# Kernel optimization log

Measured on AMD Instinct MI355X. Metric: run time of the kernel, lower is better.

## Reference

```python
import jax, jax.numpy as jnp
import numpy as np

B, S, D_MODEL, D_STATE = 4, 2048, 2048, 64
C = 8.0
SURPRISE_TEMP = 1.0
RMS_EPS = 1e-6


def _l2norm(x, eps=1e-12):
    # F.normalize(dim=-1): x / max(||x||_2, eps)
    n = jnp.sqrt(jnp.sum(x * x, axis=-1, keepdims=True))
    return x / jnp.maximum(n, eps)


def setup_inputs() -> dict:
    key = jax.random.key(0)
    ks = jax.random.split(key, 9)
    std = 0.02
    return {
        "x": jax.random.normal(ks[0], (B, S, D_MODEL), dtype=jnp.float32),
        "Wk": jax.random.normal(ks[1], (D_STATE, D_MODEL), dtype=jnp.float32) * std,
        "Wv": jax.random.normal(ks[2], (D_STATE, D_MODEL), dtype=jnp.float32) * std,
        "Wq": jax.random.normal(ks[3], (D_STATE, D_MODEL), dtype=jnp.float32) * std,
        "Wa_w": jax.random.normal(ks[4], (D_STATE, D_MODEL), dtype=jnp.float32) * std,
        "Wa_b": jnp.zeros((D_STATE,), dtype=jnp.float32),
        "lam": jax.random.uniform(ks[5], (D_STATE,), dtype=jnp.float32, minval=4.0, maxval=9.0),
        "norm_w": jnp.ones((D_STATE,), dtype=jnp.float32),
        "Wo": jax.random.normal(ks[6], (D_MODEL, D_STATE), dtype=jnp.float32) * std,
    }


def reference(x, Wk, Wv, Wq, Wa_w, Wa_b, lam, norm_w, Wo):
    b, s, _ = x.shape
    d = Wk.shape[0]
    # projections
    k = _l2norm(x @ Wk.T)                    # [B,S,d]
    v = x @ Wv.T                             # [B,S,d]
    q = _l2norm(x @ Wq.T)                    # [B,S,d]
    r = jax.nn.sigmoid(x @ Wa_w.T + Wa_b)    # [B,S,d]
    log_a = jnp.log(jax.nn.sigmoid(lam) + 1e-8)
    alpha = jnp.exp(C * r * log_a)           # [B,S,d]

    def step(H, inp):
        # H: [B, d_k, d_v]; inp tensors: [B, d]
        k_t, v_t, q_t, a_t = inp
        pred = jnp.einsum("bk,bkv->bv", q_t, H)
        err = jnp.sum((v_t - pred) ** 2, axis=-1, keepdims=True)   # [B,1]
        surprise = jax.nn.sigmoid(err / (SURPRISE_TEMP + 1e-6))    # [B,1]
        kH = jnp.einsum("bk,bkv->bv", k_t, H)
        # delta = k (x) v - k (x) (k^T H) = k (x) (v - kH)
        delta = k_t[:, :, None] * (v_t - kH)[:, None, :]           # [B,d,d]
        a = a_t[:, :, None]                                        # gate over k-dim rows
        H = a * H + (1.0 - a) * (surprise[:, :, None] * delta)
        y_t = jnp.einsum("bk,bkv->bv", q_t, H)
        return H, y_t

    H0 = jnp.zeros((b, d, d), dtype=x.dtype)
    xs = (
        jnp.swapaxes(k, 0, 1),
        jnp.swapaxes(v, 0, 1),
        jnp.swapaxes(q, 0, 1),
        jnp.swapaxes(alpha, 0, 1),
    )
    _, ys = jax.lax.scan(step, H0, xs)       # ys: [S,B,d]
    y = jnp.swapaxes(ys, 0, 1)               # [B,S,d]

    # RMSNorm (computed in fp32, cast back)
    yf = y.astype(jnp.float32)
    yn = yf * jax.lax.rsqrt(jnp.mean(yf * yf, axis=-1, keepdims=True) + RMS_EPS)
    yn = (yn * norm_w).astype(y.dtype)

    return yn @ Wo.T                          # [B,S,d_model]
```

## Files before the change

kernel.cpp:

```cpp
#include <hip/hip_runtime.h>
#include <hip/hip_bf16.h>
#include <math.h>

#define S_ 2048
#define DM_ 2048

__device__ __forceinline__ float wave_reduce_add_f32(float x) {
  float t;
  t = __int_as_float(__builtin_amdgcn_update_dpp(0, __float_as_int(x), 0x111, 0xf, 0xf, true)); x += t;
  t = __int_as_float(__builtin_amdgcn_update_dpp(0, __float_as_int(x), 0x112, 0xf, 0xf, true)); x += t;
  t = __int_as_float(__builtin_amdgcn_update_dpp(0, __float_as_int(x), 0x114, 0xf, 0xf, true)); x += t;
  t = __int_as_float(__builtin_amdgcn_update_dpp(0, __float_as_int(x), 0x118, 0xf, 0xf, true)); x += t;
  t = __int_as_float(__builtin_amdgcn_update_dpp(0, __float_as_int(x), 0x142, 0xa, 0xf, true)); x += t;
  t = __int_as_float(__builtin_amdgcn_update_dpp(0, __float_as_int(x), 0x143, 0xc, 0xf, true)); x += t;
  return __int_as_float(__builtin_amdgcn_readlane(__float_as_int(x), 63));
}

__global__ __launch_bounds__(256) void k_proj(
    const float* __restrict__ x, const float* __restrict__ Wk,
    const float* __restrict__ Wv, const float* __restrict__ Wq,
    const float* __restrict__ Wa, const float* __restrict__ Wab,
    const float* __restrict__ lam, float* __restrict__ proj,
    float* __restrict__ qwArr)
{
  __shared__ __align__(16) float xs[16 * 40];
  __shared__ __align__(16) float ws[32 * 260];
  const int tid = threadIdx.x;
  const int r0  = blockIdx.x * 16;
  const int ct  = tid & 63;
  const int rt  = tid >> 6;
  float acc[4][4];
  #pragma unroll
  for (int r = 0; r < 4; r++) { acc[r][0] = 0.f; acc[r][1] = 0.f; acc[r][2] = 0.f; acc[r][3] = 0.f; }

  const int sg = tid >> 3;
  const int sm = tid & 7;
  const float* wbase[4] = {Wk, Wv, Wq, Wa};

  for (int k0 = 0; k0 < DM_; k0 += 32) {
    if (tid < 128) {
      const int rr = tid >> 3;
      const int ko = (tid & 7) << 2;
      float4 xv = *(const float4*)(x + (size_t)(r0 + rr) * DM_ + k0 + ko);
      *(float4*)(xs + rr * 40 + ko) = xv;
    }
    #pragma unroll
    for (int p = 0; p < 8; p++) {
      const int c = sg + p * 32;
      const float* wb = wbase[p >> 1];
      const int cc = c - (p >> 1) * 64;
      float4 wv = *(const float4*)(wb + (size_t)cc * DM_ + k0 + sm * 4);
      ws[(sm * 4 + 0) * 260 + c] = wv.x;
      ws[(sm * 4 + 1) * 260 + c] = wv.y;
      ws[(sm * 4 + 2) * 260 + c] = wv.z;
      ws[(sm * 4 + 3) * 260 + c] = wv.w;
    }
    __syncthreads();
    #pragma unroll
    for (int kq = 0; kq < 8; kq++) {
      float4 xv[4];
      #pragma unroll
      for (int r = 0; r < 4; r++) xv[r] = *(const float4*)(xs + (rt * 4 + r) * 40 + kq * 4);
      #pragma unroll
      for (int i = 0; i < 4; i++) {
        const int kk = kq * 4 + i;
        float wv0 = ws[kk * 260 + ct];
        float wv1 = ws[kk * 260 + ct + 64];
        float wv2 = ws[kk * 260 + ct + 128];
        float wv3 = ws[kk * 260 + ct + 192];
        #pragma unroll
        for (int r = 0; r < 4; r++) {
          float xr = (i == 0) ? xv[r].x : (i == 1) ? xv[r].y : (i == 2) ? xv[r].z : xv[r].w;
          acc[r][0] = fmaf(xr, wv0, acc[r][0]);
          acc[r][1] = fmaf(xr, wv1, acc[r][1]);
          acc[r][2] = fmaf(xr, wv2, acc[r][2]);
          acc[r][3] = fmaf(xr, wv3, acc[r][3]);
        }
      }
    }
    __syncthreads();
  }
  float lamv = lam[ct];
  float la = logf(1.f / (1.f + expf(-lamv)) + 1e-8f);
  float bv = Wab[ct];
  #pragma unroll
  for (int r = 0; r < 4; r++) {
    float nk = wave_reduce_add_f32(acc[r][0] * acc[r][0]);
    float nq = wave_reduce_add_f32(acc[r][2] * acc[r][2]);
    nk = fmaxf(sqrtf(nk), 1e-12f);
    nq = fmaxf(sqrtf(nq), 1e-12f);
    float pre = acc[r][3] + bv;
    float rr_ = 1.f / (1.f + expf(-pre));
    float al  = expf(8.f * rr_ * la);
    float kn  = acc[r][0] / nk;
    float qn  = acc[r][2] / nq;
    float qw  = wave_reduce_add_f32(qn * (1.f - al) * kn);
    float* pr = proj + (size_t)(r0 + rt * 4 + r) * 256;
    pr[ct]        = kn;
    pr[64 + ct]   = acc[r][1];
    pr[128 + ct]  = qn;
    pr[192 + ct]  = al;
    if (ct == 0) qwArr[r0 + rt * 4 + r] = qw;
  }
}

struct KQA { float4 k[4], q[4], a[4]; float v; };

__device__ __forceinline__ void load_kqa(const float* __restrict__ slot,
                                         int w, int lane, KQA& s) {
  const float4* s4 = (const float4*)slot;
  const int o = w * 4;
  #pragma unroll
  for (int i = 0; i < 4; i++) {
    s.k[i] = s4[o + i];
    s.q[i] = s4[32 + o + i];
    s.a[i] = s4[48 + o + i];
  }
  s.v = slot[64 + lane];
}

__device__ __forceinline__ void sstep(int t, float qws, float* __restrict__ inv,
    float2* __restrict__ xchp, float* __restrict__ yb, const float* __restrict__ pb,
    float H[16], KQA& cur, KQA& nxt, float& pf, int w, int lane, int tid,
    float qwSel)
{
  inv[(((t + 2) & 3) << 8) + tid] = pf;
  pf = pb[(size_t)min(t + 4, S_ - 1) * 256 + tid];
  float4 w4[4], qa4[4];
  #pragma unroll
  for (int j = 0; j < 4; j++) {
    w4[j].x = (1.f - cur.a[j].x) * cur.k[j].x;  qa4[j].x = cur.q[j].x * cur.a[j].x;
    w4[j].y = (1.f - cur.a[j].y) * cur.k[j].y;  qa4[j].y = cur.q[j].y * cur.a[j].y;
    w4[j].z = (1.f - cur.a[j].z) * cur.k[j].z;  qa4[j].z = cur.q[j].z * cur.a[j].z;
    w4[j].w = (1.f - cur.a[j].w) * cur.k[j].w;  qa4[j].w = cur.q[j].w * cur.a[j].w;
  }
  float pA = 0.f, pB = 0.f, kA = 0.f, kB = 0.f, yA = 0.f, yB = 0.f;
  #pragma unroll
  for (int j = 0; j < 4; j++) {
    pA = fmaf(cur.q[j].x, H[4*j+0], pA); kA = fmaf(cur.k[j].x, H[4*j+0], kA); yA = fmaf(qa4[j].x, H[4*j+0], yA);
    pB = fmaf(cur.q[j].y, H[4*j+1], pB); kB = fmaf(cur.k[j].y, H[4*j+1], kB); yB = fmaf(qa4[j].y, H[4*j+1], yB);
    pA = fmaf(cur.q[j].z, H[4*j+2], pA); kA = fmaf(cur.k[j].z, H[4*j+2], kA); yA = fmaf(qa4[j].z, H[4*j+2], yA);
    pB = fmaf(cur.q[j].w, H[4*j+3], pB); kB = fmaf(cur.k[j].w, H[4*j+3], kB); yB = fmaf(qa4[j].w, H[4*j+3], yB);
  }
  xchp[(w << 6) + lane] = make_float2(pA + pB, kA + kB);
  asm volatile("s_waitcnt lgkmcnt(0)\n\ts_barrier" ::: "memory");
  float2 x0 = xchp[lane], x1 = xchp[64 + lane], x2 = xchp[128 + lane], x3 = xchp[192 + lane];
  load_kqa(inv + (((t + 1) & 3) << 8), w, lane, nxt);
  float pred = (x0.x + x1.x) + (x2.x + x3.x);
  float kh   = (x0.y + x1.y) + (x2.y + x3.y);
  float d = cur.v - pred;
  float e = wave_reduce_add_f32(d * d);
  float sg = __builtin_amdgcn_rcpf(1.f + __builtin_amdgcn_exp2f(e * -1.4426936f));
  float g = sg * (cur.v - kh);
  yb[(size_t)t * 256 + (w << 6) + lane] = (yA + yB) + qwSel * (qws * g);
  #pragma unroll
  for (int j = 0; j < 4; j++) {
    H[4*j+0] = fmaf(cur.a[j].x, H[4*j+0], w4[j].x * g);
    H[4*j+1] = fmaf(cur.a[j].y, H[4*j+1], w4[j].y * g);
    H[4*j+2] = fmaf(cur.a[j].z, H[4*j+2], w4[j].z * g);
    H[4*j+3] = fmaf(cur.a[j].w, H[4*j+3], w4[j].w * g);
  }
}

__global__ __launch_bounds__(256, 1) void k_scan(const float* __restrict__ proj,
    const float* __restrict__ qwArr, float* __restrict__ ypart)
{
  __shared__ __align__(16) float inv[4 * 256];
  __shared__ __align__(16) float2 xch[2][256];
  const int b = blockIdx.x, tid = threadIdx.x;
  const int w = tid >> 6, lane = tid & 63;
  const float* pb  = proj + (size_t)b * S_ * 256;
  const float* qwb = qwArr + (size_t)b * S_;
  float* yb = ypart + (size_t)b * S_ * 256;
  float H[16];
  #pragma unroll
  for (int j = 0; j < 16; j++) H[j] = 0.f;
  inv[tid]       = pb[tid];
  inv[256 + tid] = pb[256 + tid];
  float pfE = pb[2 * 256 + tid];
  float pfO = pb[3 * 256 + tid];
  __syncthreads();
  const float qwSel = (w == 0) ? 1.f : 0.f;
  KQA curA, curB;
  load_kqa(inv, w, lane, curA);
  for (int t0 = 0; t0 < S_; t0 += 64) {
    float qwv = qwb[t0 + lane];
    for (int tt = 0; tt < 64; tt += 2) {
      float qs0 = __int_as_float(__builtin_amdgcn_readlane(__float_as_int(qwv), tt));
      float qs1 = __int_as_float(__builtin_amdgcn_readlane(__float_as_int(qwv), tt + 1));
      sstep(t0 + tt,     qs0, inv, xch[0], yb, pb, H, curA, curB, pfE, w, lane, tid, qwSel);
      sstep(t0 + tt + 1, qs1, inv, xch[1], yb, pb, H, curB, curA, pfO, w, lane, tid, qwSel);
    }
  }
}

__global__ __launch_bounds__(256) void k_trans(const float* __restrict__ Wo,
                                               float* __restrict__ WoT) {
  int i = blockIdx.x * 256 + threadIdx.x;
  int d = i >> 11;
  int c = i & 2047;
  WoT[i] = Wo[(size_t)c * 64 + d];
}

__global__ __launch_bounds__(256) void k_out(const float* __restrict__ ypart,
    const float* __restrict__ norm_w, const float* __restrict__ WoT,
    float* __restrict__ out)
{
  __shared__ __align__(16) float yn[16 * 64];
  const int tid = threadIdx.x;
  const int r0  = blockIdx.x * 16;
  const int c0  = blockIdx.y * 512;
  {
    const int r = tid >> 4;
    const int d = (tid & 15) * 4;
    const float* yp = ypart + (size_t)(r0 + r) * 256;
    float4 y0 = *(const float4*)(yp + d);
    float4 y1 = *(const float4*)(yp + 64 + d);
    float4 y2 = *(const float4*)(yp + 128 + d);
    float4 y3 = *(const float4*)(yp + 192 + d);
    float yx = y0.x + y1.x + y2.x + y3.x;
    float yy = y0.y + y1.y + y2.y + y3.y;
    float yz = y0.z + y1.z + y2.z + y3.z;
    float yw = y0.w + y1.w + y2.w + y3.w;
    float sq = yx * yx + yy * yy + yz * yz + yw * yw;
    sq += __shfl_xor(sq, 1, 64);
    sq += __shfl_xor(sq, 2, 64);
    sq += __shfl_xor(sq, 4, 64);
    sq += __shfl_xor(sq, 8, 64);
    float rms = rsqrtf(sq * (1.f / 64.f) + 1e-6f);
    float4 nw = *(const float4*)(norm_w + d);
    yn[r * 64 + d + 0] = yx * rms * nw.x;
    yn[r * 64 + d + 1] = yy * rms * nw.y;
    yn[r * 64 + d + 2] = yz * rms * nw.z;
    yn[r * 64 + d + 3] = yw * rms * nw.w;
  }
  __syncthreads();
  const int ctq = tid & 127;
  const int rt  = tid >> 7;
  float acc[8][4];
  #pragma unroll
  for (int r = 0; r < 8; r++) { acc[r][0] = 0.f; acc[r][1] = 0.f; acc[r][2] = 0.f; acc[r][3] = 0.f; }
  #pragma unroll 8
  for (int d = 0; d < 64; d++) {
    float4 wv = *(const float4*)(WoT + (size_t)d * 2048 + c0 + ctq * 4);
    #pragma unroll
    for (int r = 0; r < 8; r++) {
      float yv = yn[(rt * 8 + r) * 64 + d];
      acc[r][0] = fmaf(yv, wv.x, acc[r][0]);
      acc[r][1] = fmaf(yv, wv.y, acc[r][1]);
      acc[r][2] = fmaf(yv, wv.z, acc[r][2]);
      acc[r][3] = fmaf(yv, wv.w, acc[r][3]);
    }
  }
  #pragma unroll
  for (int r = 0; r < 8; r++) {
    float4 o; o.x = acc[r][0]; o.y = acc[r][1]; o.z = acc[r][2]; o.w = acc[r][3];
    *(float4*)(out + (size_t)(r0 + rt * 8 + r) * 2048 + c0 + ctq * 4) = o;
  }
}

extern "C" void kernel_launch(void* const* d_in, const int* in_sizes, int n_in,
                              void* d_out, int out_size, void* d_ws, size_t ws_size,
                              hipStream_t stream) {
  const float* x   = (const float*)d_in[0];
  const float* Wk  = (const float*)d_in[1];
  const float* Wv  = (const float*)d_in[2];
  const float* Wq  = (const float*)d_in[3];
  const float* Wa  = (const float*)d_in[4];
  const float* Wab = (const float*)d_in[5];
  const float* lam = (const float*)d_in[6];
  const float* nw  = (const float*)d_in[7];
  const float* Wo  = (const float*)d_in[8];
  float* out = (float*)d_out;

  float* wsf   = (float*)d_ws;
  float* proj  = wsf;
  float* ypart = wsf + 2097152;
  float* WoT   = wsf + 4194304;
  float* qwArr = wsf + 4325376;

  k_trans<<<dim3(512), dim3(256), 0, stream>>>(Wo, WoT);
  k_proj <<<dim3(512), dim3(256), 0, stream>>>(x, Wk, Wv, Wq, Wa, Wab, lam, proj, qwArr);
  k_scan <<<dim3(4),   dim3(256), 0, stream>>>(proj, qwArr, ypart);
  k_out  <<<dim3(512, 4), dim3(256), 0, stream>>>(ypart, nw, WoT, out);
}
```

Baseline: 1.375 ms.

## Precompute next-step dot products to take H update off the serial critical path

Rewrites the scan recurrence so that the q·H, k·H and output dot products for step t+1 are computed from the pre-update state H_t, using the next step's gates. The rank-1 correction from the current step's update is applied as scalar coefficients that a new k_coef kernel precomputes per timestep. The intent is to shorten the per-step dependency chain in the latency-bound 4-block scan, so the cross-wave exchange and barrier overlap with the state update. In exchange it adds an extra kernel launch, more FMAs per step and an algebraic reordering that can change rounding.

```diff
diff --git a/kernel.cpp b/kernel.cpp
--- a/kernel.cpp
+++ b/kernel.cpp
@@ -14,6 +14,10 @@
   t = __int_as_float(__builtin_amdgcn_update_dpp(0, __float_as_int(x), 0x142, 0xa, 0xf, true)); x += t;
   t = __int_as_float(__builtin_amdgcn_update_dpp(0, __float_as_int(x), 0x143, 0xc, 0xf, true)); x += t;
   return __int_as_float(__builtin_amdgcn_readlane(__float_as_int(x), 63));
+}
+
+__device__ __forceinline__ float rdlane(float x, int l) {
+  return __int_as_float(__builtin_amdgcn_readlane(__float_as_int(x), l));
 }
 
 __global__ __launch_bounds__(256) void k_proj(
@@ -104,6 +108,29 @@
   }
 }
 
+__global__ __launch_bounds__(256) void k_coef(const float* __restrict__ proj,
+                                              float* __restrict__ scArr)
+{
+  const int row  = blockIdx.x * 4 + (threadIdx.x >> 6);
+  const int lane = threadIdx.x & 63;
+  const int t = row & (S_ - 1);
+  const float* pr = proj + (size_t)row * 256;
+  float kn = pr[lane];
+  float qn = pr[128 + lane];
+  float al = pr[192 + lane];
+  float wprev = 0.f;
+  if (t > 0) {
+    const float* pp = pr - 256;
+    wprev = (1.f - pp[192 + lane]) * pp[lane];
+  }
+  float w  = (1.f - al) * kn;
+  float cq = wave_reduce_add_f32(qn * wprev);
+  float ck = wave_reduce_add_f32(kn * wprev);
+  float cy = wave_reduce_add_f32(qn * al * wprev);
+  float qw = wave_reduce_add_f32(qn * w);
+  if (lane == 0) *(float4*)(scArr + (size_t)row * 4) = make_float4(cq, ck, cy, qw);
+}
+
 struct KQA { float4 k[4], q[4], a[4]; float v; };
 
 __device__ __forceinline__ void load_kqa(const float* __restrict__ slot,
@@ -119,62 +146,70 @@
   s.v = slot[64 + lane];
 }
 
-__device__ __forceinline__ void sstep(int t, float qws, float* __restrict__ inv,
-    float2* __restrict__ xchp, float* __restrict__ yb, const float* __restrict__ pb,
-    float H[16], KQA& cur, KQA& nxt, float& pf, int w, int lane, int tid,
-    float qwSel)
-{
-  inv[(((t + 2) & 3) << 8) + tid] = pf;
-  pf = pb[(size_t)min(t + 4, S_ - 1) * 256 + tid];
-  float4 w4[4], qa4[4];
-  #pragma unroll
-  for (int j = 0; j < 4; j++) {
-    w4[j].x = (1.f - cur.a[j].x) * cur.k[j].x;  qa4[j].x = cur.q[j].x * cur.a[j].x;
-    w4[j].y = (1.f - cur.a[j].y) * cur.k[j].y;  qa4[j].y = cur.q[j].y * cur.a[j].y;
-    w4[j].z = (1.f - cur.a[j].z) * cur.k[j].z;  qa4[j].z = cur.q[j].z * cur.a[j].z;
-    w4[j].w = (1.f - cur.a[j].w) * cur.k[j].w;  qa4[j].w = cur.q[j].w * cur.a[j].w;
-  }
-  float pA = 0.f, pB = 0.f, kA = 0.f, kB = 0.f, yA = 0.f, yB = 0.f;
-  #pragma unroll
-  for (int j = 0; j < 4; j++) {
-    pA = fmaf(cur.q[j].x, H[4*j+0], pA); kA = fmaf(cur.k[j].x, H[4*j+0], kA); yA = fmaf(qa4[j].x, H[4*j+0], yA);
-    pB = fmaf(cur.q[j].y, H[4*j+1], pB); kB = fmaf(cur.k[j].y, H[4*j+1], kB); yB = fmaf(qa4[j].y, H[4*j+1], yB);
-    pA = fmaf(cur.q[j].z, H[4*j+2], pA); kA = fmaf(cur.k[j].z, H[4*j+2], kA); yA = fmaf(qa4[j].z, H[4*j+2], yA);
-    pB = fmaf(cur.q[j].w, H[4*j+3], pB); kB = fmaf(cur.k[j].w, H[4*j+3], kB); yB = fmaf(qa4[j].w, H[4*j+3], yB);
-  }
-  xchp[(w << 6) + lane] = make_float2(pA + pB, kA + kB);
-  asm volatile("s_waitcnt lgkmcnt(0)\n\ts_barrier" ::: "memory");
-  float2 x0 = xchp[lane], x1 = xchp[64 + lane], x2 = xchp[128 + lane], x3 = xchp[192 + lane];
-  load_kqa(inv + (((t + 1) & 3) << 8), w, lane, nxt);
-  float pred = (x0.x + x1.x) + (x2.x + x3.x);
-  float kh   = (x0.y + x1.y) + (x2.y + x3.y);
+__device__ __forceinline__ void sstep(int t, float4 sc, float* __restrict__ inv,
+    const float2* __restrict__ xchR, float2* __restrict__ xchW,
+    float* __restrict__ yb, const float* __restrict__ pb,
+    float H[16], KQA& cur, KQA& nxt, float& d3c, float& gP,
+    float& pf, int w, int lane, int tid, float qwSel)
+{
+  float2 x0 = xchR[lane], x1 = xchR[64 + lane], x2 = xchR[128 + lane], x3 = xchR[192 + lane];
+  float D1f = (x0.x + x1.x) + (x2.x + x3.x);
+  float D2f = (x0.y + x1.y) + (x2.y + x3.y);
+  float pred = fmaf(sc.x, gP, D1f);
+  float kh   = fmaf(sc.y, gP, D2f);
   float d = cur.v - pred;
   float e = wave_reduce_add_f32(d * d);
   float sg = __builtin_amdgcn_rcpf(1.f + __builtin_amdgcn_exp2f(e * -1.4426936f));
   float g = sg * (cur.v - kh);
-  yb[(size_t)t * 256 + (w << 6) + lane] = (yA + yB) + qwSel * (qws * g);
+  yb[(size_t)t * 256 + tid] = d3c + qwSel * fmaf(sc.z, gP, sc.w * g);
+  inv[(((t + 2) & 3) << 8) + tid] = pf;
+  pf = pb[(size_t)min(t + 4, S_ - 1) * 256 + tid];
+  load_kqa(inv + (((t + 1) & 3) << 8), w, lane, nxt);
+  float dA = 0.f, dB = 0.f, kA = 0.f, kB = 0.f, yA = 0.f, yB = 0.f;
   #pragma unroll
   for (int j = 0; j < 4; j++) {
-    H[4*j+0] = fmaf(cur.a[j].x, H[4*j+0], w4[j].x * g);
-    H[4*j+1] = fmaf(cur.a[j].y, H[4*j+1], w4[j].y * g);
-    H[4*j+2] = fmaf(cur.a[j].z, H[4*j+2], w4[j].z * g);
-    H[4*j+3] = fmaf(cur.a[j].w, H[4*j+3], w4[j].w * g);
-  }
+    float c1, c2, c3;
+    c1 = nxt.q[j].x * cur.a[j].x; c2 = nxt.k[j].x * cur.a[j].x; c3 = c1 * nxt.a[j].x;
+    dA = fmaf(c1, H[4*j+0], dA); kA = fmaf(c2, H[4*j+0], kA); yA = fmaf(c3, H[4*j+0], yA);
+    c1 = nxt.q[j].y * cur.a[j].y; c2 = nxt.k[j].y * cur.a[j].y; c3 = c1 * nxt.a[j].y;
+    dB = fmaf(c1, H[4*j+1], dB); kB = fmaf(c2, H[4*j+1], kB); yB = fmaf(c3, H[4*j+1], yB);
+    c1 = nxt.q[j].z * cur.a[j].z; c2 = nxt.k[j].z * cur.a[j].z; c3 = c1 * nxt.a[j].z;
+    dA = fmaf(c1, H[4*j+2], dA); kA = fmaf(c2, H[4*j+2], kA); yA = fmaf(c3, H[4*j+2], yA);
+    c1 = nxt.q[j].w * cur.a[j].w; c2 = nxt.k[j].w * cur.a[j].w; c3 = c1 * nxt.a[j].w;
+    dB = fmaf(c1, H[4*j+3], dB); kB = fmaf(c2, H[4*j+3], kB); yB = fmaf(c3, H[4*j+3], yB);
+  }
+  d3c = yA + yB;
+  xchW[(w << 6) + lane] = make_float2(dA + dB, kA + kB);
+  #pragma unroll
+  for (int j = 0; j < 4; j++) {
+    float wx = (1.f - cur.a[j].x) * cur.k[j].x;
+    float wy = (1.f - cur.a[j].y) * cur.k[j].y;
+    float wz = (1.f - cur.a[j].z) * cur.k[j].z;
+    float ww = (1.f - cur.a[j].w) * cur.k[j].w;
+    H[4*j+0] = fmaf(cur.a[j].x, H[4*j+0], wx * g);
+    H[4*j+1] = fmaf(cur.a[j].y, H[4*j+1], wy * g);
+    H[4*j+2] = fmaf(cur.a[j].z, H[4*j+2], wz * g);
+    H[4*j+3] = fmaf(cur.a[j].w, H[4*j+3], ww * g);
+  }
+  asm volatile("s_waitcnt lgkmcnt(0)\n\ts_barrier" ::: "memory");
+  gP = g;
 }
 
 __global__ __launch_bounds__(256, 1) void k_scan(const float* __restrict__ proj,
-    const float* __restrict__ qwArr, float* __restrict__ ypart)
+    const float* __restrict__ scArr, float* __restrict__ ypart)
 {
   __shared__ __align__(16) float inv[4 * 256];
   __shared__ __align__(16) float2 xch[2][256];
   const int b = blockIdx.x, tid = threadIdx.x;
   const int w = tid >> 6, lane = tid & 63;
   const float* pb  = proj + (size_t)b * S_ * 256;
-  const float* qwb = qwArr + (size_t)b * S_;
+  const float4* scb = (const float4*)scArr + (size_t)b * S_;
   float* yb = ypart + (size_t)b * S_ * 256;
   float H[16];
   #pragma unroll
   for (int j = 0; j < 16; j++) H[j] = 0.f;
+  float gP = 0.f, d3c = 0.f;
+  xch[0][tid] = make_float2(0.f, 0.f);
   inv[tid]       = pb[tid];
   inv[256 + tid] = pb[256 + tid];
   float pfE = pb[2 * 256 + tid];
@@ -184,12 +219,14 @@
   KQA curA, curB;
   load_kqa(inv, w, lane, curA);
   for (int t0 = 0; t0 < S_; t0 += 64) {
-    float qwv = qwb[t0 + lane];
+    float4 scv = scb[t0 + lane];
     for (int tt = 0; tt < 64; tt += 2) {
-      float qs0 = __int_as_float(__builtin_amdgcn_readlane(__float_as_int(qwv), tt));
-      float qs1 = __int_as_float(__builtin_amdgcn_readlane(__float_as_int(qwv), tt + 1));
-      sstep(t0 + tt,     qs0, inv, xch[0], yb, pb, H, curA, curB, pfE, w, lane, tid, qwSel);
-      sstep(t0 + tt + 1, qs1, inv, xch[1], yb, pb, H, curB, curA, pfO, w, lane, tid, qwSel);
+      float4 s0 = make_float4(rdlane(scv.x, tt),     rdlane(scv.y, tt),
+                              rdlane(scv.z, tt),     rdlane(scv.w, tt));
+      float4 s1 = make_float4(rdlane(scv.x, tt + 1), rdlane(scv.y, tt + 1),
+                              rdlane(scv.z, tt + 1), rdlane(scv.w, tt + 1));
+      sstep(t0 + tt,     s0, inv, xch[0], xch[1], yb, pb, H, curA, curB, d3c, gP, pfE, w, lane, tid, qwSel);
+      sstep(t0 + tt + 1, s1, inv, xch[1], xch[0], yb, pb, H, curB, curA, d3c, gP, pfO, w, lane, tid, qwSel);
     }
   }
 }
@@ -278,9 +315,11 @@
   float* ypart = wsf + 2097152;
   float* WoT   = wsf + 4194304;
   float* qwArr = wsf + 4325376;
+  float* scArr = wsf + 4333568;
 
   k_trans<<<dim3(512), dim3(256), 0, stream>>>(Wo, WoT);
   k_proj <<<dim3(512), dim3(256), 0, stream>>>(x, Wk, Wv, Wq, Wa, Wab, lam, proj, qwArr);
-  k_scan <<<dim3(4),   dim3(256), 0, stream>>>(proj, qwArr, ypart);
+  k_coef <<<dim3(2048), dim3(256), 0, stream>>>(proj, scArr);
+  k_scan <<<dim3(4),   dim3(256), 0, stream>>>(proj, scArr, ypart);
   k_out  <<<dim3(512, 4), dim3(256), 0, stream>>>(ypart, nw, WoT, out);
 }
```

Result: slower. 1.524 ms (+10.9%).

## Process two scan steps per barrier using precomputed cross-step coefficients

Applied to the files above, without the earlier changes.

Restructures the sequential delta-rule scan to advance two timesteps per block barrier instead of one. A new k_coef kernel precomputes scalar dot-product coefficients between adjacent steps' k/q/a rows, so the dependence of step t+1 on the not-yet-applied updates of step t (and of the previous pair) is folded in algebraically. The cost targeted is the per-step barrier and shared-memory exchange latency on the serial critical path. In exchange there is an extra kernel launch, more FMAs per thread per step, an 8-slot input ring, and the results may differ slightly in floating-point rounding.

```diff
diff --git a/kernel.cpp b/kernel.cpp
--- a/kernel.cpp
+++ b/kernel.cpp
@@ -4,6 +4,7 @@
 
 #define S_ 2048
 #define DM_ 2048
+#define NPH (S_ / 2)
 
 __device__ __forceinline__ float wave_reduce_add_f32(float x) {
   float t;
@@ -104,93 +105,181 @@
   }
 }
 
-struct KQA { float4 k[4], q[4], a[4]; float v; };
-
-__device__ __forceinline__ void load_kqa(const float* __restrict__ slot,
-                                         int w, int lane, KQA& s) {
-  const float4* s4 = (const float4*)slot;
+__global__ __launch_bounds__(256) void k_coef(const float* __restrict__ proj,
+                                              float* __restrict__ scArr)
+{
+  const int P    = blockIdx.x * 4 + (threadIdx.x >> 6);
+  const int lane = threadIdx.x & 63;
+  const int p    = P & (NPH - 1);
+  const int t    = p * 2;
+  const float* pr0 = proj + ((size_t)(P >> 10) * S_ + t) * 256;
+  const float* pr1 = pr0 + 256;
+  float k0 = pr0[lane], q0 = pr0[128 + lane], a0 = pr0[192 + lane];
+  float k1 = pr1[lane], q1 = pr1[128 + lane], a1 = pr1[192 + lane];
+  float w0 = (1.f - a0) * k0;
+  float w1 = (1.f - a1) * k1;
+  float W0p = 0.f, W1p = 0.f;
+  if (p > 0) {
+    const float* pm1 = pr0 - 256;
+    const float* pm2 = pr0 - 512;
+    float am1 = pm1[192 + lane], km1 = pm1[lane];
+    float am2 = pm2[192 + lane], km2 = pm2[lane];
+    float wm2 = (1.f - am2) * km2;
+    W0p = am1 * wm2;
+    W1p = (1.f - am1) * km1;
+  }
+  float q0a0 = q0 * a0;
+  float q1a0 = q1 * a0;
+  float k1a0 = k1 * a0;
+  float q1a1a0 = q1a0 * a1;
+  float sq00 = wave_reduce_add_f32(q0 * W0p);
+  float sq01 = wave_reduce_add_f32(q0 * W1p);
+  float sk00 = wave_reduce_add_f32(k0 * W0p);
+  float sk01 = wave_reduce_add_f32(k0 * W1p);
+  float sy00 = wave_reduce_add_f32(q0a0 * W0p);
+  float sy01 = wave_reduce_add_f32(q0a0 * W1p);
+  float qw0  = wave_reduce_add_f32(q0 * w0);
+  float sq10 = wave_reduce_add_f32(q1a0 * W0p);
+  float sq11 = wave_reduce_add_f32(q1a0 * W1p);
+  float sk10 = wave_reduce_add_f32(k1a0 * W0p);
+  float sk11 = wave_reduce_add_f32(k1a0 * W1p);
+  float sy10 = wave_reduce_add_f32(q1a1a0 * W0p);
+  float sy11 = wave_reduce_add_f32(q1a1a0 * W1p);
+  float cqi  = wave_reduce_add_f32(q1 * w0);
+  float cki  = wave_reduce_add_f32(k1 * w0);
+  float cyi  = wave_reduce_add_f32(q1 * a1 * w0);
+  float qw1  = wave_reduce_add_f32(q1 * w1);
+  if (lane == 0) {
+    float4* so = (float4*)(scArr + (size_t)P * 20);
+    so[0] = make_float4(sq00, sq01, sk00, sk01);
+    so[1] = make_float4(sy00, sy01, qw0, sq10);
+    so[2] = make_float4(sq11, sk10, sk11, sy10);
+    so[3] = make_float4(sy11, cqi, cki, cyi);
+    so[4] = make_float4(qw1, 0.f, 0.f, 0.f);
+  }
+}
+
+struct Rows { float4 q[2][4], k[2][4], a[2][4]; };
+
+__device__ __forceinline__ void load_rows(const float* __restrict__ inv,
+                                          int sA, int sB, int w, Rows& R) {
+  const float4* r0 = (const float4*)(inv + (sA << 8));
+  const float4* r1 = (const float4*)(inv + (sB << 8));
   const int o = w * 4;
   #pragma unroll
   for (int i = 0; i < 4; i++) {
-    s.k[i] = s4[o + i];
-    s.q[i] = s4[32 + o + i];
-    s.a[i] = s4[48 + o + i];
-  }
-  s.v = slot[64 + lane];
-}
-
-__device__ __forceinline__ void sstep(int t, float qws, float* __restrict__ inv,
-    float2* __restrict__ xchp, float* __restrict__ yb, const float* __restrict__ pb,
-    float H[16], KQA& cur, KQA& nxt, float& pf, int w, int lane, int tid,
-    float qwSel)
-{
-  inv[(((t + 2) & 3) << 8) + tid] = pf;
-  pf = pb[(size_t)min(t + 4, S_ - 1) * 256 + tid];
-  float4 w4[4], qa4[4];
+    R.k[0][i] = r0[o + i];       R.k[1][i] = r1[o + i];
+    R.q[0][i] = r0[32 + o + i];  R.q[1][i] = r1[32 + o + i];
+    R.a[0][i] = r0[48 + o + i];  R.a[1][i] = r1[48 + o + i];
+  }
+}
+
+#define PHASE_DOT(J, C, HI) { \
+  float A_  = CUR.a[1][J].C * CUR.a[0][J].C; \
+  float c1_ = NXT.q[0][J].C * A_; \
+  float c2_ = NXT.k[0][J].C * A_; \
+  float c3_ = c1_ * NXT.a[0][J].C; \
+  float am_ = NXT.a[0][J].C * A_; \
+  float f1_ = NXT.q[1][J].C * am_; \
+  float f2_ = NXT.k[1][J].C * am_; \
+  float f3_ = f1_ * NXT.a[1][J].C; \
+  float h_  = H[4*(J)+(HI)]; \
+  D1n = fmaf(c1_, h_, D1n); D2n = fmaf(c2_, h_, D2n); D3n = fmaf(c3_, h_, D3n); \
+  D1m = fmaf(f1_, h_, D1m); D2m = fmaf(f2_, h_, D2m); D3m = fmaf(f3_, h_, D3m); }
+
+#define PHASE_HUP(J, C, HI) { \
+  float a0_ = CUR.a[0][J].C, a1_ = CUR.a[1][J].C; \
+  float w0_ = (1.f - a0_) * CUR.k[0][J].C; \
+  float w1_ = (1.f - a1_) * CUR.k[1][J].C; \
+  float tm_ = fmaf(w1_, g1, (a1_ * w0_) * g0); \
+  H[4*(J)+(HI)] = fmaf(a1_ * a0_, H[4*(J)+(HI)], tm_); }
+
+__device__ __forceinline__ void pstep(int t,
+    const float4* __restrict__ sc, float4* __restrict__ scn,
+    const float4* __restrict__ scb,
+    float* __restrict__ inv, const float4* __restrict__ xchR,
+    float4* __restrict__ xchW, float* __restrict__ yb,
+    const float* __restrict__ pb, float H[16], Rows& CUR, Rows& NXT,
+    float& d3c0, float& d3c1, float& g0p, float& g1p,
+    float& pfE, float& pfO, int w, int lane, int tid, float qwSel)
+{
+  {
+    const float4* sp = scb + (size_t)min((t >> 1) + 1, NPH - 1) * 5;
+    scn[0] = sp[0]; scn[1] = sp[1]; scn[2] = sp[2]; scn[3] = sp[3]; scn[4] = sp[4];
+  }
+  float v0 = inv[((t & 7) << 8) + 64 + lane];
+  float v1 = inv[(((t + 1) & 7) << 8) + 64 + lane];
+  load_rows(inv, (t + 2) & 7, (t + 3) & 7, w, NXT);
+  float4 x0 = xchR[lane], x1 = xchR[64 + lane], x2 = xchR[128 + lane], x3 = xchR[192 + lane];
+  float D1  = (x0.x + x1.x) + (x2.x + x3.x);
+  float D2  = (x0.y + x1.y) + (x2.y + x3.y);
+  float D1b = (x0.z + x1.z) + (x2.z + x3.z);
+  float D2b = (x0.w + x1.w) + (x2.w + x3.w);
+  float pred0 = fmaf(sc[0].x, g0p, fmaf(sc[0].y, g1p, D1));
+  float kh0   = fmaf(sc[0].z, g0p, fmaf(sc[0].w, g1p, D2));
+  float d0 = v0 - pred0;
+  float e0 = wave_reduce_add_f32(d0 * d0);
+  float sg0 = __builtin_amdgcn_rcpf(1.f + __builtin_amdgcn_exp2f(e0 * -1.4426936f));
+  float g0 = sg0 * (v0 - kh0);
+  yb[(size_t)t * 256 + tid] = d3c0 + qwSel * fmaf(sc[1].x, g0p, fmaf(sc[1].y, g1p, sc[1].z * g0));
+  float pred1 = fmaf(sc[3].y, g0, fmaf(sc[1].w, g0p, fmaf(sc[2].x, g1p, D1b)));
+  float kh1   = fmaf(sc[3].z, g0, fmaf(sc[2].y, g0p, fmaf(sc[2].z, g1p, D2b)));
+  float d1 = v1 - pred1;
+  float e1 = wave_reduce_add_f32(d1 * d1);
+  float sg1 = __builtin_amdgcn_rcpf(1.f + __builtin_amdgcn_exp2f(e1 * -1.4426936f));
+  float g1 = sg1 * (v1 - kh1);
+  yb[(size_t)(t + 1) * 256 + tid] =
+      d3c1 + qwSel * fmaf(sc[2].w, g0p, fmaf(sc[3].x, g1p, fmaf(sc[3].w, g0, sc[4].x * g1)));
+  float D1n = 0.f, D2n = 0.f, D3n = 0.f, D1m = 0.f, D2m = 0.f, D3m = 0.f;
   #pragma unroll
   for (int j = 0; j < 4; j++) {
-    w4[j].x = (1.f - cur.a[j].x) * cur.k[j].x;  qa4[j].x = cur.q[j].x * cur.a[j].x;
-    w4[j].y = (1.f - cur.a[j].y) * cur.k[j].y;  qa4[j].y = cur.q[j].y * cur.a[j].y;
-    w4[j].z = (1.f - cur.a[j].z) * cur.k[j].z;  qa4[j].z = cur.q[j].z * cur.a[j].z;
-    w4[j].w = (1.f - cur.a[j].w) * cur.k[j].w;  qa4[j].w = cur.q[j].w * cur.a[j].w;
-  }
-  float pA = 0.f, pB = 0.f, kA = 0.f, kB = 0.f, yA = 0.f, yB = 0.f;
+    PHASE_DOT(j, x, 0); PHASE_DOT(j, y, 1); PHASE_DOT(j, z, 2); PHASE_DOT(j, w, 3);
+  }
+  d3c0 = D3n;
+  d3c1 = D3m;
+  xchW[(w << 6) + lane] = make_float4(D1n, D2n, D1m, D2m);
   #pragma unroll
   for (int j = 0; j < 4; j++) {
-    pA = fmaf(cur.q[j].x, H[4*j+0], pA); kA = fmaf(cur.k[j].x, H[4*j+0], kA); yA = fmaf(qa4[j].x, H[4*j+0], yA);
-    pB = fmaf(cur.q[j].y, H[4*j+1], pB); kB = fmaf(cur.k[j].y, H[4*j+1], kB); yB = fmaf(qa4[j].y, H[4*j+1], yB);
-    pA = fmaf(cur.q[j].z, H[4*j+2], pA); kA = fmaf(cur.k[j].z, H[4*j+2], kA); yA = fmaf(qa4[j].z, H[4*j+2], yA);
-    pB = fmaf(cur.q[j].w, H[4*j+3], pB); kB = fmaf(cur.k[j].w, H[4*j+3], kB); yB = fmaf(qa4[j].w, H[4*j+3], yB);
-  }
-  xchp[(w << 6) + lane] = make_float2(pA + pB, kA + kB);
+    PHASE_HUP(j, x, 0); PHASE_HUP(j, y, 1); PHASE_HUP(j, z, 2); PHASE_HUP(j, w, 3);
+  }
+  inv[(((t + 6) & 7) << 8) + tid] = pfE;
+  inv[(((t + 7) & 7) << 8) + tid] = pfO;
+  pfE = pb[(size_t)min(t + 8, S_ - 1) * 256 + tid];
+  pfO = pb[(size_t)min(t + 9, S_ - 1) * 256 + tid];
   asm volatile("s_waitcnt lgkmcnt(0)\n\ts_barrier" ::: "memory");
-  float2 x0 = xchp[lane], x1 = xchp[64 + lane], x2 = xchp[128 + lane], x3 = xchp[192 + lane];
-  load_kqa(inv + (((t + 1) & 3) << 8), w, lane, nxt);
-  float pred = (x0.x + x1.x) + (x2.x + x3.x);
-  float kh   = (x0.y + x1.y) + (x2.y + x3.y);
-  float d = cur.v - pred;
-  float e = wave_reduce_add_f32(d * d);
-  float sg = __builtin_amdgcn_rcpf(1.f + __builtin_amdgcn_exp2f(e * -1.4426936f));
-  float g = sg * (cur.v - kh);
-  yb[(size_t)t * 256 + (w << 6) + lane] = (yA + yB) + qwSel * (qws * g);
-  #pragma unroll
-  for (int j = 0; j < 4; j++) {
-    H[4*j+0] = fmaf(cur.a[j].x, H[4*j+0], w4[j].x * g);
-    H[4*j+1] = fmaf(cur.a[j].y, H[4*j+1], w4[j].y * g);
-    H[4*j+2] = fmaf(cur.a[j].z, H[4*j+2], w4[j].z * g);
-    H[4*j+3] = fmaf(cur.a[j].w, H[4*j+3], w4[j].w * g);
-  }
+  g0p = g0; g1p = g1;
 }
 
 __global__ __launch_bounds__(256, 1) void k_scan(const float* __restrict__ proj,
-    const float* __restrict__ qwArr, float* __restrict__ ypart)
-{
-  __shared__ __align__(16) float inv[4 * 256];
-  __shared__ __align__(16) float2 xch[2][256];
+    const float* __restrict__ scArr, float* __restrict__ ypart)
+{
+  __shared__ __align__(16) float inv[8 * 256];
+  __shared__ __align__(16) float4 xch[2][256];
   const int b = blockIdx.x, tid = threadIdx.x;
   const int w = tid >> 6, lane = tid & 63;
-  const float* pb  = proj + (size_t)b * S_ * 256;
-  const float* qwb = qwArr + (size_t)b * S_;
+  const float* pb = proj + (size_t)b * S_ * 256;
+  const float4* scb = (const float4*)scArr + (size_t)b * NPH * 5;
   float* yb = ypart + (size_t)b * S_ * 256;
   float H[16];
   #pragma unroll
   for (int j = 0; j < 16; j++) H[j] = 0.f;
-  inv[tid]       = pb[tid];
-  inv[256 + tid] = pb[256 + tid];
-  float pfE = pb[2 * 256 + tid];
-  float pfO = pb[3 * 256 + tid];
+  float d3c0 = 0.f, d3c1 = 0.f, g0p = 0.f, g1p = 0.f;
+  xch[0][tid] = make_float4(0.f, 0.f, 0.f, 0.f);
+  #pragma unroll
+  for (int i = 0; i < 6; i++) inv[i * 256 + tid] = pb[i * 256 + tid];
+  float pfE = pb[6 * 256 + tid];
+  float pfO = pb[7 * 256 + tid];
+  float4 scA[5], scB[5];
+  { const float4* sp = scb; scA[0]=sp[0]; scA[1]=sp[1]; scA[2]=sp[2]; scA[3]=sp[3]; scA[4]=sp[4]; }
   __syncthreads();
+  Rows RA, RB;
+  load_rows(inv, 0, 1, w, RA);
   const float qwSel = (w == 0) ? 1.f : 0.f;
-  KQA curA, curB;
-  load_kqa(inv, w, lane, curA);
-  for (int t0 = 0; t0 < S_; t0 += 64) {
-    float qwv = qwb[t0 + lane];
-    for (int tt = 0; tt < 64; tt += 2) {
-      float qs0 = __int_as_float(__builtin_amdgcn_readlane(__float_as_int(qwv), tt));
-      float qs1 = __int_as_float(__builtin_amdgcn_readlane(__float_as_int(qwv), tt + 1));
-      sstep(t0 + tt,     qs0, inv, xch[0], yb, pb, H, curA, curB, pfE, w, lane, tid, qwSel);
-      sstep(t0 + tt + 1, qs1, inv, xch[1], yb, pb, H, curB, curA, pfO, w, lane, tid, qwSel);
-    }
+  for (int t = 0; t < S_; t += 4) {
+    pstep(t,     scA, scB, scb, inv, xch[0], xch[1], yb, pb, H, RA, RB,
+          d3c0, d3c1, g0p, g1p, pfE, pfO, w, lane, tid, qwSel);
+    pstep(t + 2, scB, scA, scb, inv, xch[1], xch[0], yb, pb, H, RB, RA,
+          d3c0, d3c1, g0p, g1p, pfE, pfO, w, lane, tid, qwSel);
   }
 }
 
@@ -278,9 +367,11 @@
   float* ypart = wsf + 2097152;
   float* WoT   = wsf + 4194304;
   float* qwArr = wsf + 4325376;
+  float* scArr = wsf + 4333568;
 
   k_trans<<<dim3(512), dim3(256), 0, stream>>>(Wo, WoT);
   k_proj <<<dim3(512), dim3(256), 0, stream>>>(x, Wk, Wv, Wq, Wa, Wab, lam, proj, qwArr);
-  k_scan <<<dim3(4),   dim3(256), 0, stream>>>(proj, qwArr, ypart);
+  k_coef <<<dim3(1024), dim3(256), 0, stream>>>(proj, scArr);
+  k_scan <<<dim3(4),   dim3(256), 0, stream>>>(proj, scArr, ypart);
   k_out  <<<dim3(512, 4), dim3(256), 0, stream>>>(ypart, nw, WoT, out);
 }
```

After: 1.572 ms. 1.14x slower.

## Split scan state across eight waves and reduce y output in-kernel

Applied to the files above, without the earlier changes.

The recurrent scan kernel now runs 512 threads (eight waves), each holding 8 rows of the 64x64 state instead of 16. This halves the per-thread serial work per timestep. The y partial sums are exchanged through shared memory along with pred and kH, and wave 0 writes a single reduced y row, so the output kernel no longer sums four partials. The cost is a larger cross-wave exchange (eight float4 reads per step), a barrier across more waves each step, and only half the threads staging the next inputs.

```diff
diff --git a/kernel.cpp b/kernel.cpp
--- a/kernel.cpp
+++ b/kernel.cpp
@@ -14,6 +14,10 @@
   t = __int_as_float(__builtin_amdgcn_update_dpp(0, __float_as_int(x), 0x142, 0xa, 0xf, true)); x += t;
   t = __int_as_float(__builtin_amdgcn_update_dpp(0, __float_as_int(x), 0x143, 0xc, 0xf, true)); x += t;
   return __int_as_float(__builtin_amdgcn_readlane(__float_as_int(x), 63));
+}
+
+__device__ __forceinline__ float rdlane(float x, int l) {
+  return __int_as_float(__builtin_amdgcn_readlane(__float_as_int(x), l));
 }
 
 __global__ __launch_bounds__(256) void k_proj(
@@ -104,14 +108,14 @@
   }
 }
 
-struct KQA { float4 k[4], q[4], a[4]; float v; };
-
-__device__ __forceinline__ void load_kqa(const float* __restrict__ slot,
-                                         int w, int lane, KQA& s) {
+struct KQA8 { float4 k[2], q[2], a[2]; float v; };
+
+__device__ __forceinline__ void load_kqa8(const float* __restrict__ slot,
+                                          int w, int lane, KQA8& s) {
   const float4* s4 = (const float4*)slot;
-  const int o = w * 4;
-  #pragma unroll
-  for (int i = 0; i < 4; i++) {
+  const int o = w * 2;
+  #pragma unroll
+  for (int i = 0; i < 2; i++) {
     s.k[i] = s4[o + i];
     s.q[i] = s4[32 + o + i];
     s.a[i] = s4[48 + o + i];
@@ -120,41 +124,47 @@
 }
 
 __device__ __forceinline__ void sstep(int t, float qws, float* __restrict__ inv,
-    float2* __restrict__ xchp, float* __restrict__ yb, const float* __restrict__ pb,
-    float H[16], KQA& cur, KQA& nxt, float& pf, int w, int lane, int tid,
-    float qwSel)
-{
-  inv[(((t + 2) & 3) << 8) + tid] = pf;
-  pf = pb[(size_t)min(t + 4, S_ - 1) * 256 + tid];
-  float4 w4[4], qa4[4];
-  #pragma unroll
-  for (int j = 0; j < 4; j++) {
+    float4* __restrict__ xchp, float* __restrict__ yb, const float* __restrict__ pb,
+    float H[8], KQA8& cur, KQA8& nxt, float& pf, int w, int lane, int tid,
+    bool stager)
+{
+  if (stager) {
+    inv[(((t + 2) & 3) << 8) + tid] = pf;
+    pf = pb[(size_t)min(t + 4, S_ - 1) * 256 + tid];
+  }
+  float4 w4[2], qa4[2];
+  #pragma unroll
+  for (int j = 0; j < 2; j++) {
     w4[j].x = (1.f - cur.a[j].x) * cur.k[j].x;  qa4[j].x = cur.q[j].x * cur.a[j].x;
     w4[j].y = (1.f - cur.a[j].y) * cur.k[j].y;  qa4[j].y = cur.q[j].y * cur.a[j].y;
     w4[j].z = (1.f - cur.a[j].z) * cur.k[j].z;  qa4[j].z = cur.q[j].z * cur.a[j].z;
     w4[j].w = (1.f - cur.a[j].w) * cur.k[j].w;  qa4[j].w = cur.q[j].w * cur.a[j].w;
   }
-  float pA = 0.f, pB = 0.f, kA = 0.f, kB = 0.f, yA = 0.f, yB = 0.f;
-  #pragma unroll
-  for (int j = 0; j < 4; j++) {
+  float pA = 0.f, kA = 0.f, yA = 0.f;
+  #pragma unroll
+  for (int j = 0; j < 2; j++) {
     pA = fmaf(cur.q[j].x, H[4*j+0], pA); kA = fmaf(cur.k[j].x, H[4*j+0], kA); yA = fmaf(qa4[j].x, H[4*j+0], yA);
-    pB = fmaf(cur.q[j].y, H[4*j+1], pB); kB = fmaf(cur.k[j].y, H[4*j+1], kB); yB = fmaf(qa4[j].y, H[4*j+1], yB);
+    pA = fmaf(cur.q[j].y, H[4*j+1], pA); kA = fmaf(cur.k[j].y, H[4*j+1], kA); yA = fmaf(qa4[j].y, H[4*j+1], yA);
     pA = fmaf(cur.q[j].z, H[4*j+2], pA); kA = fmaf(cur.k[j].z, H[4*j+2], kA); yA = fmaf(qa4[j].z, H[4*j+2], yA);
-    pB = fmaf(cur.q[j].w, H[4*j+3], pB); kB = fmaf(cur.k[j].w, H[4*j+3], kB); yB = fmaf(qa4[j].w, H[4*j+3], yB);
-  }
-  xchp[(w << 6) + lane] = make_float2(pA + pB, kA + kB);
+    pA = fmaf(cur.q[j].w, H[4*j+3], pA); kA = fmaf(cur.k[j].w, H[4*j+3], kA); yA = fmaf(qa4[j].w, H[4*j+3], yA);
+  }
+  xchp[(w << 6) + lane] = make_float4(pA, kA, yA, 0.f);
   asm volatile("s_waitcnt lgkmcnt(0)\n\ts_barrier" ::: "memory");
-  float2 x0 = xchp[lane], x1 = xchp[64 + lane], x2 = xchp[128 + lane], x3 = xchp[192 + lane];
-  load_kqa(inv + (((t + 1) & 3) << 8), w, lane, nxt);
-  float pred = (x0.x + x1.x) + (x2.x + x3.x);
-  float kh   = (x0.y + x1.y) + (x2.y + x3.y);
+  float4 e0 = xchp[lane],        e1 = xchp[64 + lane],  e2 = xchp[128 + lane], e3 = xchp[192 + lane];
+  float4 e4 = xchp[256 + lane],  e5 = xchp[320 + lane], e6 = xchp[384 + lane], e7 = xchp[448 + lane];
+  load_kqa8(inv + (((t + 1) & 3) << 8), w, lane, nxt);
+  float pred = ((e0.x + e1.x) + (e2.x + e3.x)) + ((e4.x + e5.x) + (e6.x + e7.x));
+  float kh   = ((e0.y + e1.y) + (e2.y + e3.y)) + ((e4.y + e5.y) + (e6.y + e7.y));
   float d = cur.v - pred;
   float e = wave_reduce_add_f32(d * d);
   float sg = __builtin_amdgcn_rcpf(1.f + __builtin_amdgcn_exp2f(e * -1.4426936f));
   float g = sg * (cur.v - kh);
-  yb[(size_t)t * 256 + (w << 6) + lane] = (yA + yB) + qwSel * (qws * g);
-  #pragma unroll
-  for (int j = 0; j < 4; j++) {
+  if (w == 0) {
+    float yfull = ((e0.z + e1.z) + (e2.z + e3.z)) + ((e4.z + e5.z) + (e6.z + e7.z));
+    yb[(size_t)t * 64 + lane] = fmaf(qws, g, yfull);
+  }
+  #pragma unroll
+  for (int j = 0; j < 2; j++) {
     H[4*j+0] = fmaf(cur.a[j].x, H[4*j+0], w4[j].x * g);
     H[4*j+1] = fmaf(cur.a[j].y, H[4*j+1], w4[j].y * g);
     H[4*j+2] = fmaf(cur.a[j].z, H[4*j+2], w4[j].z * g);
@@ -162,34 +172,36 @@
   }
 }
 
-__global__ __launch_bounds__(256, 1) void k_scan(const float* __restrict__ proj,
+__global__ __launch_bounds__(512, 1) void k_scan(const float* __restrict__ proj,
     const float* __restrict__ qwArr, float* __restrict__ ypart)
 {
   __shared__ __align__(16) float inv[4 * 256];
-  __shared__ __align__(16) float2 xch[2][256];
+  __shared__ __align__(16) float4 xch[2][512];
   const int b = blockIdx.x, tid = threadIdx.x;
   const int w = tid >> 6, lane = tid & 63;
   const float* pb  = proj + (size_t)b * S_ * 256;
   const float* qwb = qwArr + (size_t)b * S_;
-  float* yb = ypart + (size_t)b * S_ * 256;
-  float H[16];
-  #pragma unroll
-  for (int j = 0; j < 16; j++) H[j] = 0.f;
-  inv[tid]       = pb[tid];
-  inv[256 + tid] = pb[256 + tid];
-  float pfE = pb[2 * 256 + tid];
-  float pfO = pb[3 * 256 + tid];
+  float* yb = ypart + (size_t)b * S_ * 64;
+  float H[8];
+  #pragma unroll
+  for (int j = 0; j < 8; j++) H[j] = 0.f;
+  inv[tid] = pb[tid];
+  const bool stager = (tid < 256);
+  float pfE = 0.f, pfO = 0.f;
+  if (stager) {
+    pfE = pb[2 * 256 + tid];
+    pfO = pb[3 * 256 + tid];
+  }
   __syncthreads();
-  const float qwSel = (w == 0) ? 1.f : 0.f;
-  KQA curA, curB;
-  load_kqa(inv, w, lane, curA);
+  KQA8 curA, curB;
+  load_kqa8(inv, w, lane, curA);
   for (int t0 = 0; t0 < S_; t0 += 64) {
     float qwv = qwb[t0 + lane];
     for (int tt = 0; tt < 64; tt += 2) {
-      float qs0 = __int_as_float(__builtin_amdgcn_readlane(__float_as_int(qwv), tt));
-      float qs1 = __int_as_float(__builtin_amdgcn_readlane(__float_as_int(qwv), tt + 1));
-      sstep(t0 + tt,     qs0, inv, xch[0], yb, pb, H, curA, curB, pfE, w, lane, tid, qwSel);
-      sstep(t0 + tt + 1, qs1, inv, xch[1], yb, pb, H, curB, curA, pfO, w, lane, tid, qwSel);
+      float qs0 = rdlane(qwv, tt);
+      float qs1 = rdlane(qwv, tt + 1);
+      sstep(t0 + tt,     qs0, inv, xch[0], yb, pb, H, curA, curB, pfE, w, lane, tid, stager);
+      sstep(t0 + tt + 1, qs1, inv, xch[1], yb, pb, H, curB, curA, pfO, w, lane, tid, stager);
     }
   }
 }
@@ -213,15 +225,9 @@
   {
     const int r = tid >> 4;
     const int d = (tid & 15) * 4;
-    const float* yp = ypart + (size_t)(r0 + r) * 256;
+    const float* yp = ypart + (size_t)(r0 + r) * 64;
     float4 y0 = *(const float4*)(yp + d);
-    float4 y1 = *(const float4*)(yp + 64 + d);
-    float4 y2 = *(const float4*)(yp + 128 + d);
-    float4 y3 = *(const float4*)(yp + 192 + d);
-    float yx = y0.x + y1.x + y2.x + y3.x;
-    float yy = y0.y + y1.y + y2.y + y3.y;
-    float yz = y0.z + y1.z + y2.z + y3.z;
-    float yw = y0.w + y1.w + y2.w + y3.w;
+    float yx = y0.x, yy = y0.y, yz = y0.z, yw = y0.w;
     float sq = yx * yx + yy * yy + yz * yz + yw * yw;
     sq += __shfl_xor(sq, 1, 64);
     sq += __shfl_xor(sq, 2, 64);
@@ -276,11 +282,11 @@
   float* wsf   = (float*)d_ws;
   float* proj  = wsf;
   float* ypart = wsf + 2097152;
-  float* WoT   = wsf + 4194304;
-  float* qwArr = wsf + 4325376;
+  float* WoT   = wsf + 2621440;
+  float* qwArr = wsf + 2752512;
 
   k_trans<<<dim3(512), dim3(256), 0, stream>>>(Wo, WoT);
   k_proj <<<dim3(512), dim3(256), 0, stream>>>(x, Wk, Wv, Wq, Wa, Wab, lam, proj, qwArr);
-  k_scan <<<dim3(4),   dim3(256), 0, stream>>>(proj, qwArr, ypart);
+  k_scan <<<dim3(4),   dim3(512), 0, stream>>>(proj, qwArr, ypart);
   k_out  <<<dim3(512, 4), dim3(256), 0, stream>>>(ypart, nw, WoT, out);
 }
```

Measured after the change: 1.712 ms. 24.6% more time.
